# Kernel tuning notes

Measured on AMD Instinct MI355X. Metric: run time of the kernel, lower is better.

The kernel has to match this reference:

```python
import jax, jax.numpy as jnp
import numpy as np
from jax import lax

B, S, I, H = 16, 2048, 256, 512


def setup_inputs() -> dict:
    key = jax.random.key(0)
    k = jax.random.split(key, 5)
    s0 = 1.0 / np.sqrt(I + H)
    s1 = 1.0 / np.sqrt(H + H)
    return {
        "x": jax.random.normal(k[0], (B, S, I), dtype=jnp.float32),
        "W0": jax.random.uniform(k[1], (4 * H, I + H), minval=-s0, maxval=s0, dtype=jnp.float32),
        "b0": jax.random.uniform(k[2], (4 * H,), minval=-s0, maxval=s0, dtype=jnp.float32),
        "W1": jax.random.uniform(k[3], (4 * H, H + H), minval=-s1, maxval=s1, dtype=jnp.float32),
        "b1": jax.random.uniform(k[4], (4 * H,), minval=-s1, maxval=s1, dtype=jnp.float32),
    }


def _cell(xt, h, c, W, b):
    # gates: [B, 4H] = cat(xt, h) @ W^T + b
    g = jnp.concatenate([xt, h], axis=1) @ W.T + b
    i_t, f_t, c_tilde, o_t = jnp.split(g, 4, axis=1)
    c_new = jax.nn.sigmoid(f_t) * c + jax.nn.sigmoid(i_t) * jnp.tanh(c_tilde)
    h_new = jax.nn.sigmoid(o_t) * jnp.tanh(c_new)
    return h_new, c_new


def reference(x, W0, b0, W1, b1):
    b, s, _ = x.shape
    hdim = W0.shape[0] // 4
    z = jnp.zeros((b, hdim), dtype=x.dtype)
    init = (z, z, z, z)  # (h0, c0, h1, c1)

    def step(carry, xt):
        h0, c0, h1, c1 = carry
        h0, c0 = _cell(xt, h0, c0, W0, b0)
        h1, c1 = _cell(h0, h1, c1, W1, b1)
        return (h0, c0, h1, c1), h1

    (h0, c0, h1, c1), ys = lax.scan(step, init, jnp.swapaxes(x, 0, 1))
    outputs = jnp.swapaxes(ys, 0, 1)  # [B, S, H] (batch_first=True)
    h = jnp.stack([h0, h1], axis=0)  # [num_layers, B, H]
    c = jnp.stack([c0, c1], axis=0)
    return outputs, (h, c)
```

## Files before the change

### kernel.cpp

```cpp
#include <hip/hip_runtime.h>
#include <hip/hip_bf16.h>


#define BB 16
#define SS 2048
#define II 256
#define HH 512
#define NG0 32
#define NG1 32
#define BHH (BB * HH)
#define OUT_H_OFF (BB * SS * HH)
#define OUT_C_OFF (OUT_H_OFF + 2 * BB * HH)

typedef __bf16 bf16x8_t __attribute__((ext_vector_type(8)));
typedef float f32x4_t __attribute__((ext_vector_type(4)));

union b128u { uint64_t u[2]; bf16x8_t v; };

__device__ __forceinline__ float sigmoidf_(float x) { return 1.f / (1.f + __expf(-x)); }
__device__ __forceinline__ float tanhf_(float x) { return 1.f - 2.f / (__expf(2.f * x) + 1.f); }

__device__ __forceinline__ uint64_t cload64(const void* p) {
    return __hip_atomic_load((const uint64_t*)p, __ATOMIC_RELAXED, __HIP_MEMORY_SCOPE_AGENT);
}
__device__ __forceinline__ bf16x8_t cload_frag(const __bf16* p) {
    b128u r;
    r.u[0] = cload64(p);
    r.u[1] = cload64(p + 4);
    return r.v;
}
__device__ __forceinline__ void cstore_bf16(__bf16* p, float v) {
    __bf16 b = (__bf16)v;
    unsigned short u;
    __builtin_memcpy(&u, &b, 2);
    __hip_atomic_store((unsigned short*)p, u, __ATOMIC_RELAXED, __HIP_MEMORY_SCOPE_AGENT);
}

__device__ __forceinline__ void spin2(const int* f0, int T0, const int* f1, int T1) {
    const int lidx = threadIdx.x & 63;
    const int* p = (lidx < 32) ? (f0 + lidx) : (f1 + (lidx - 32));
    const int tgt = (lidx < 32) ? T0 : T1;
    while (true) {
        int v = __hip_atomic_load(p, __ATOMIC_RELAXED, __HIP_MEMORY_SCOPE_AGENT);
        if (__all(v >= tgt)) break;
    }
    __builtin_amdgcn_sched_barrier(0);
    asm volatile("" ::: "memory");
}

__device__ __forceinline__ bf16x8_t cvt8(const float* p) {
    f32x4_t a = *reinterpret_cast<const f32x4_t*>(p);
    f32x4_t b = *reinterpret_cast<const f32x4_t*>(p + 4);
    bf16x8_t r;
    r[0] = (__bf16)a[0]; r[1] = (__bf16)a[1];
    r[2] = (__bf16)a[2]; r[3] = (__bf16)a[3];
    r[4] = (__bf16)b[0]; r[5] = (__bf16)b[1];
    r[6] = (__bf16)b[2]; r[7] = (__bf16)b[3];
    return r;
}

#define MFMA(A, B, C) __builtin_amdgcn_mfma_f32_16x16x32_bf16((A), (B), (C), 0, 0, 0)

__global__ __launch_bounds__(256, 1) void lstm2_persistent(
    const float* __restrict__ x,
    const float* __restrict__ W0,
    const float* __restrict__ b0,
    const float* __restrict__ W1,
    const float* __restrict__ b1,
    float* __restrict__ out,
    int* flag0, int* flag1,
    __bf16* h0buf, __bf16* h1buf)
{
    const int tid = threadIdx.x;
    const int w   = tid >> 6;
    const int l   = tid & 63;
    const int cc  = l & 15;
    const int kg  = l >> 4;
    const int ew_b = tid >> 4;
    const int ew_u = tid & 15;

    __shared__ float gate_s[4][16][17];
    float cstate = 0.f;

    if (blockIdx.x < NG0) {
        const int blk   = blockIdx.x;
        const int ubase = blk * 16;
        const int gcol  = w * HH + ubase + cc;
        const float* wrow = W0 + (size_t)gcol * (II + HH);
        bf16x8_t wf[24];
#pragma unroll
        for (int kk = 0; kk < 24; ++kk)
            wf[kk] = cvt8(wrow + kk * 32 + kg * 8);
        const float bias  = b0[gcol];
        const float* xrow = x + (size_t)cc * SS * II;
        bf16x8_t xf[8];
#pragma unroll
        for (int kk = 0; kk < 8; ++kk)
            xf[kk] = cvt8(xrow + kk * 32 + kg * 8);
        __syncthreads();

        for (int t = 0; t < SS; ++t) {
            f32x4_t a0 = {0.f,0.f,0.f,0.f}, a1 = a0, a2 = a0, a3 = a0;
            a0 = MFMA(xf[0], wf[0], a0); a1 = MFMA(xf[1], wf[1], a1);
            a2 = MFMA(xf[2], wf[2], a2); a3 = MFMA(xf[3], wf[3], a3);
            a0 = MFMA(xf[4], wf[4], a0); a1 = MFMA(xf[5], wf[5], a1);
            a2 = MFMA(xf[6], wf[6], a2); a3 = MFMA(xf[7], wf[7], a3);

            spin2(flag0, t, flag1, t - 1);

            if (t > 0) {
                const __bf16* hp = h0buf + ((t - 1) & 1) * BHH + cc * HH + kg * 8;
#pragma unroll
                for (int kk = 0; kk < 16; kk += 4) {
                    a0 = MFMA(cload_frag(hp + (kk + 0) * 32), wf[8 + kk + 0], a0);
                    a1 = MFMA(cload_frag(hp + (kk + 1) * 32), wf[8 + kk + 1], a1);
                    a2 = MFMA(cload_frag(hp + (kk + 2) * 32), wf[8 + kk + 2], a2);
                    a3 = MFMA(cload_frag(hp + (kk + 3) * 32), wf[8 + kk + 3], a3);
                }
            }
            f32x4_t acc = (a0 + a1) + (a2 + a3);
#pragma unroll
            for (int r = 0; r < 4; ++r)
                gate_s[w][cc][kg * 4 + r] = acc[r] + bias;

            if (t + 1 < SS) {
                const float* xr = xrow + (size_t)(t + 1) * II;
#pragma unroll
                for (int kk = 0; kk < 8; ++kk)
                    xf[kk] = cvt8(xr + kk * 32 + kg * 8);
            }
            __syncthreads();
            {
                const float gi = gate_s[0][ew_u][ew_b];
                const float gf = gate_s[1][ew_u][ew_b];
                const float gg = gate_s[2][ew_u][ew_b];
                const float go = gate_s[3][ew_u][ew_b];
                const float cn = sigmoidf_(gf) * cstate + sigmoidf_(gi) * tanhf_(gg);
                const float hn = sigmoidf_(go) * tanhf_(cn);
                cstate = cn;
                cstore_bf16(h0buf + (t & 1) * BHH + ew_b * HH + ubase + ew_u, hn);
                if (t == SS - 1) {
                    out[OUT_H_OFF + ew_b * HH + ubase + ew_u] = hn;
                    out[OUT_C_OFF + ew_b * HH + ubase + ew_u] = cn;
                }
            }
            asm volatile("s_waitcnt vmcnt(0)" ::: "memory");
            __syncthreads();
            if (tid == 0)
                __hip_atomic_store(flag0 + blk, t + 1, __ATOMIC_RELAXED,
                                   __HIP_MEMORY_SCOPE_AGENT);
        }
    } else {
        const int blk   = blockIdx.x - NG0;
        const int ubase = blk * 16;
        const int gcol  = w * HH + ubase + cc;
        const float* wrow = W1 + (size_t)gcol * (2 * HH);
        bf16x8_t wf[32];
#pragma unroll
        for (int kk = 0; kk < 32; ++kk)
            wf[kk] = cvt8(wrow + kk * 32 + kg * 8);
        const float bias = b1[gcol];
        __syncthreads();

        for (int t = 0; t < SS; ++t) {
            f32x4_t a0 = {0.f,0.f,0.f,0.f}, a1 = a0, a2 = a0, a3 = a0;
            spin2(flag1, t, flag1, t);
            if (t > 0) {
                const __bf16* h1p = h1buf + ((t - 1) & 1) * BHH + cc * HH + kg * 8;
#pragma unroll
                for (int kk = 0; kk < 16; kk += 4) {
                    a0 = MFMA(cload_frag(h1p + (kk + 0) * 32), wf[16 + kk + 0], a0);
                    a1 = MFMA(cload_frag(h1p + (kk + 1) * 32), wf[16 + kk + 1], a1);
                    a2 = MFMA(cload_frag(h1p + (kk + 2) * 32), wf[16 + kk + 2], a2);
                    a3 = MFMA(cload_frag(h1p + (kk + 3) * 32), wf[16 + kk + 3], a3);
                }
            }
            spin2(flag0, t + 1, flag0, t + 1);
            {
                const __bf16* h0c = h0buf + (t & 1) * BHH + cc * HH + kg * 8;
#pragma unroll
                for (int kk = 0; kk < 16; kk += 4) {
                    a0 = MFMA(cload_frag(h0c + (kk + 0) * 32), wf[kk + 0], a0);
                    a1 = MFMA(cload_frag(h0c + (kk + 1) * 32), wf[kk + 1], a1);
                    a2 = MFMA(cload_frag(h0c + (kk + 2) * 32), wf[kk + 2], a2);
                    a3 = MFMA(cload_frag(h0c + (kk + 3) * 32), wf[kk + 3], a3);
                }
            }
            f32x4_t acc = (a0 + a1) + (a2 + a3);
#pragma unroll
            for (int r = 0; r < 4; ++r)
                gate_s[w][cc][kg * 4 + r] = acc[r] + bias;
            __syncthreads();
            {
                const float gi = gate_s[0][ew_u][ew_b];
                const float gf = gate_s[1][ew_u][ew_b];
                const float gg = gate_s[2][ew_u][ew_b];
                const float go = gate_s[3][ew_u][ew_b];
                const float cn = sigmoidf_(gf) * cstate + sigmoidf_(gi) * tanhf_(gg);
                const float hn = sigmoidf_(go) * tanhf_(cn);
                cstate = cn;
                cstore_bf16(h1buf + (t & 1) * BHH + ew_b * HH + ubase + ew_u, hn);
                out[((size_t)ew_b * SS + t) * HH + ubase + ew_u] = hn;
                if (t == SS - 1) {
                    out[OUT_H_OFF + (BB + ew_b) * HH + ubase + ew_u] = hn;
                    out[OUT_C_OFF + (BB + ew_b) * HH + ubase + ew_u] = cn;
                }
            }
            asm volatile("s_waitcnt vmcnt(0)" ::: "memory");
            __syncthreads();
            if (tid == 0)
                __hip_atomic_store(flag1 + blk, t + 1, __ATOMIC_RELAXED,
                                   __HIP_MEMORY_SCOPE_AGENT);
        }
    }
}

extern "C" void kernel_launch(void* const* d_in, const int* in_sizes, int n_in,
                              void* d_out, int out_size, void* d_ws, size_t ws_size,
                              hipStream_t stream) {
    const float* x  = (const float*)d_in[0];
    const float* W0 = (const float*)d_in[1];
    const float* b0 = (const float*)d_in[2];
    const float* W1 = (const float*)d_in[3];
    const float* b1 = (const float*)d_in[4];
    float* out = (float*)d_out;

    char* ws = (char*)d_ws;
    int* flag0 = (int*)ws;
    int* flag1 = (int*)(ws + 128);
    __bf16* h0buf = (__bf16*)(ws + 4096);
    __bf16* h1buf = (__bf16*)(ws + 4096 + 32768);

    hipMemsetAsync(ws, 0, 256, stream);

    hipLaunchKernelGGL(lstm2_persistent, dim3(NG0 + NG1), dim3(256), 0, stream,
                       x, W0, b0, W1, b1, out, flag0, flag1, h0buf, h1buf);
}
```

Measured before the change: 21.26 ms.

## Fuse both LSTM layers into one block per unit slice with skewed pipeline

Merges the layer-0 and layer-1 persistent blocks into 32 blocks of 512 threads. Waves 0-3 compute layer 0 at step t while waves 4-7 compute layer 1 at step t-1, so both layers share one grid-wide barrier per step instead of two dependent flag waits. Per-block flags are padded to separate cache lines and polled by one wave, and the next x load is issued before the spin and converted to bf16 afterwards to hide its latency. The price is a longer per-step critical path inside each block, since both layers' MFMA work and elementwise updates must finish before the block signals.

```diff
diff --git a/kernel.cpp b/kernel.cpp
--- a/kernel.cpp
+++ b/kernel.cpp
@@ -6,8 +6,7 @@
 #define SS 2048
 #define II 256
 #define HH 512
-#define NG0 32
-#define NG1 32
+#define NBLK 32
 #define BHH (BB * HH)
 #define OUT_H_OFF (BB * SS * HH)
 #define OUT_C_OFF (OUT_H_OFF + 2 * BB * HH)
@@ -36,21 +35,7 @@
     __hip_atomic_store((unsigned short*)p, u, __ATOMIC_RELAXED, __HIP_MEMORY_SCOPE_AGENT);
 }
 
-__device__ __forceinline__ void spin2(const int* f0, int T0, const int* f1, int T1) {
-    const int lidx = threadIdx.x & 63;
-    const int* p = (lidx < 32) ? (f0 + lidx) : (f1 + (lidx - 32));
-    const int tgt = (lidx < 32) ? T0 : T1;
-    while (true) {
-        int v = __hip_atomic_load(p, __ATOMIC_RELAXED, __HIP_MEMORY_SCOPE_AGENT);
-        if (__all(v >= tgt)) break;
-    }
-    __builtin_amdgcn_sched_barrier(0);
-    asm volatile("" ::: "memory");
-}
-
-__device__ __forceinline__ bf16x8_t cvt8(const float* p) {
-    f32x4_t a = *reinterpret_cast<const f32x4_t*>(p);
-    f32x4_t b = *reinterpret_cast<const f32x4_t*>(p + 4);
+__device__ __forceinline__ bf16x8_t pack8(f32x4_t a, f32x4_t b) {
     bf16x8_t r;
     r[0] = (__bf16)a[0]; r[1] = (__bf16)a[1];
     r[2] = (__bf16)a[2]; r[3] = (__bf16)a[3];
@@ -58,126 +43,129 @@
     r[6] = (__bf16)b[2]; r[7] = (__bf16)b[3];
     return r;
 }
+__device__ __forceinline__ bf16x8_t cvt8(const float* p) {
+    return pack8(*reinterpret_cast<const f32x4_t*>(p),
+                 *reinterpret_cast<const f32x4_t*>(p + 4));
+}
 
 #define MFMA(A, B, C) __builtin_amdgcn_mfma_f32_16x16x32_bf16((A), (B), (C), 0, 0, 0)
 
-__global__ __launch_bounds__(256, 1) void lstm2_persistent(
+__global__ __launch_bounds__(512, 1) void lstm2_fused(
     const float* __restrict__ x,
     const float* __restrict__ W0,
     const float* __restrict__ b0,
     const float* __restrict__ W1,
     const float* __restrict__ b1,
     float* __restrict__ out,
-    int* flag0, int* flag1,
+    int* flags,
     __bf16* h0buf, __bf16* h1buf)
 {
-    const int tid = threadIdx.x;
-    const int w   = tid >> 6;
-    const int l   = tid & 63;
-    const int cc  = l & 15;
-    const int kg  = l >> 4;
-    const int ew_b = tid >> 4;
-    const int ew_u = tid & 15;
-
-    __shared__ float gate_s[4][16][17];
-    float cstate = 0.f;
-
-    if (blockIdx.x < NG0) {
-        const int blk   = blockIdx.x;
-        const int ubase = blk * 16;
-        const int gcol  = w * HH + ubase + cc;
+    const int tid  = threadIdx.x;
+    const int w    = tid >> 6;
+    const int l    = tid & 63;
+    const int cc   = l & 15;
+    const int kg   = l >> 4;
+    const int gate = w & 3;
+    const bool isL0 = (w < 4);
+    const int blk   = blockIdx.x;
+    const int ubase = blk * 16;
+    const int gcol  = gate * HH + ubase + cc;
+
+    const int half = tid >> 8;
+    const int eb   = (tid >> 4) & 15;
+    const int eu   = tid & 15;
+
+    __shared__ float g0s[4][16][17];
+    __shared__ float g1s[4][16][17];
+
+    bf16x8_t wf[32];
+    float    bias;
+    bf16x8_t xf[8];
+    const float* xrow = x + (size_t)cc * SS * II;
+
+    if (isL0) {
         const float* wrow = W0 + (size_t)gcol * (II + HH);
-        bf16x8_t wf[24];
 #pragma unroll
         for (int kk = 0; kk < 24; ++kk)
             wf[kk] = cvt8(wrow + kk * 32 + kg * 8);
-        const float bias  = b0[gcol];
-        const float* xrow = x + (size_t)cc * SS * II;
-        bf16x8_t xf[8];
+        bias = b0[gcol];
 #pragma unroll
         for (int kk = 0; kk < 8; ++kk)
             xf[kk] = cvt8(xrow + kk * 32 + kg * 8);
-        __syncthreads();
-
-        for (int t = 0; t < SS; ++t) {
-            f32x4_t a0 = {0.f,0.f,0.f,0.f}, a1 = a0, a2 = a0, a3 = a0;
+    } else {
+        const float* wrow = W1 + (size_t)gcol * (2 * HH);
+#pragma unroll
+        for (int kk = 0; kk < 32; ++kk)
+            wf[kk] = cvt8(wrow + kk * 32 + kg * 8);
+        bias = b1[gcol];
+    }
+
+    float cstate = 0.f;
+    __syncthreads();
+
+    for (int t = 0; t <= SS; ++t) {
+        f32x4_t a0 = {0.f, 0.f, 0.f, 0.f}, a1 = a0, a2 = a0, a3 = a0;
+        f32x4_t xraw[16];
+
+        if (isL0 && t < SS) {
             a0 = MFMA(xf[0], wf[0], a0); a1 = MFMA(xf[1], wf[1], a1);
             a2 = MFMA(xf[2], wf[2], a2); a3 = MFMA(xf[3], wf[3], a3);
             a0 = MFMA(xf[4], wf[4], a0); a1 = MFMA(xf[5], wf[5], a1);
             a2 = MFMA(xf[6], wf[6], a2); a3 = MFMA(xf[7], wf[7], a3);
-
-            spin2(flag0, t, flag1, t - 1);
-
-            if (t > 0) {
-                const __bf16* hp = h0buf + ((t - 1) & 1) * BHH + cc * HH + kg * 8;
-#pragma unroll
-                for (int kk = 0; kk < 16; kk += 4) {
-                    a0 = MFMA(cload_frag(hp + (kk + 0) * 32), wf[8 + kk + 0], a0);
-                    a1 = MFMA(cload_frag(hp + (kk + 1) * 32), wf[8 + kk + 1], a1);
-                    a2 = MFMA(cload_frag(hp + (kk + 2) * 32), wf[8 + kk + 2], a2);
-                    a3 = MFMA(cload_frag(hp + (kk + 3) * 32), wf[8 + kk + 3], a3);
-                }
-            }
-            f32x4_t acc = (a0 + a1) + (a2 + a3);
-#pragma unroll
-            for (int r = 0; r < 4; ++r)
-                gate_s[w][cc][kg * 4 + r] = acc[r] + bias;
-
             if (t + 1 < SS) {
                 const float* xr = xrow + (size_t)(t + 1) * II;
 #pragma unroll
-                for (int kk = 0; kk < 8; ++kk)
-                    xf[kk] = cvt8(xr + kk * 32 + kg * 8);
-            }
-            __syncthreads();
-            {
-                const float gi = gate_s[0][ew_u][ew_b];
-                const float gf = gate_s[1][ew_u][ew_b];
-                const float gg = gate_s[2][ew_u][ew_b];
-                const float go = gate_s[3][ew_u][ew_b];
-                const float cn = sigmoidf_(gf) * cstate + sigmoidf_(gi) * tanhf_(gg);
-                const float hn = sigmoidf_(go) * tanhf_(cn);
-                cstate = cn;
-                cstore_bf16(h0buf + (t & 1) * BHH + ew_b * HH + ubase + ew_u, hn);
-                if (t == SS - 1) {
-                    out[OUT_H_OFF + ew_b * HH + ubase + ew_u] = hn;
-                    out[OUT_C_OFF + ew_b * HH + ubase + ew_u] = cn;
-                }
-            }
-            asm volatile("s_waitcnt vmcnt(0)" ::: "memory");
-            __syncthreads();
-            if (tid == 0)
-                __hip_atomic_store(flag0 + blk, t + 1, __ATOMIC_RELAXED,
-                                   __HIP_MEMORY_SCOPE_AGENT);
-        }
-    } else {
-        const int blk   = blockIdx.x - NG0;
-        const int ubase = blk * 16;
-        const int gcol  = w * HH + ubase + cc;
-        const float* wrow = W1 + (size_t)gcol * (2 * HH);
-        bf16x8_t wf[32];
-#pragma unroll
-        for (int kk = 0; kk < 32; ++kk)
-            wf[kk] = cvt8(wrow + kk * 32 + kg * 8);
-        const float bias = b1[gcol];
+                for (int kk = 0; kk < 8; ++kk) {
+                    xraw[2 * kk]     = *reinterpret_cast<const f32x4_t*>(xr + kk * 32 + kg * 8);
+                    xraw[2 * kk + 1] = *reinterpret_cast<const f32x4_t*>(xr + kk * 32 + kg * 8 + 4);
+                }
+            }
+        }
+
+        if (w == 0) {
+            const int* p = flags + (l & 31) * 32;
+            while (true) {
+                int v = __hip_atomic_load(p, __ATOMIC_RELAXED, __HIP_MEMORY_SCOPE_AGENT);
+                if (__all(v >= t)) break;
+            }
+        }
         __syncthreads();
 
-        for (int t = 0; t < SS; ++t) {
-            f32x4_t a0 = {0.f,0.f,0.f,0.f}, a1 = a0, a2 = a0, a3 = a0;
-            spin2(flag1, t, flag1, t);
-            if (t > 0) {
-                const __bf16* h1p = h1buf + ((t - 1) & 1) * BHH + cc * HH + kg * 8;
-#pragma unroll
-                for (int kk = 0; kk < 16; kk += 4) {
-                    a0 = MFMA(cload_frag(h1p + (kk + 0) * 32), wf[16 + kk + 0], a0);
-                    a1 = MFMA(cload_frag(h1p + (kk + 1) * 32), wf[16 + kk + 1], a1);
-                    a2 = MFMA(cload_frag(h1p + (kk + 2) * 32), wf[16 + kk + 2], a2);
-                    a3 = MFMA(cload_frag(h1p + (kk + 3) * 32), wf[16 + kk + 3], a3);
-                }
-            }
-            spin2(flag0, t + 1, flag0, t + 1);
-            {
-                const __bf16* h0c = h0buf + (t & 1) * BHH + cc * HH + kg * 8;
+        if (isL0) {
+            if (t < SS) {
+                if (t + 1 < SS) {
+#pragma unroll
+                    for (int kk = 0; kk < 8; ++kk)
+                        xf[kk] = pack8(xraw[2 * kk], xraw[2 * kk + 1]);
+                }
+                if (t > 0) {
+                    const __bf16* hp = h0buf + ((t - 1) & 1) * BHH + cc * HH + kg * 8;
+#pragma unroll
+                    for (int kk = 0; kk < 16; kk += 4) {
+                        a0 = MFMA(cload_frag(hp + (kk + 0) * 32), wf[8 + kk + 0], a0);
+                        a1 = MFMA(cload_frag(hp + (kk + 1) * 32), wf[8 + kk + 1], a1);
+                        a2 = MFMA(cload_frag(hp + (kk + 2) * 32), wf[8 + kk + 2], a2);
+                        a3 = MFMA(cload_frag(hp + (kk + 3) * 32), wf[8 + kk + 3], a3);
+                    }
+                }
+                f32x4_t acc = (a0 + a1) + (a2 + a3);
+#pragma unroll
+                for (int r = 0; r < 4; ++r)
+                    g0s[gate][cc][kg * 4 + r] = acc[r] + bias;
+            }
+        } else {
+            if (t >= 1) {
+                if (t >= 2) {
+                    const __bf16* h1p = h1buf + ((t - 2) & 1) * BHH + cc * HH + kg * 8;
+#pragma unroll
+                    for (int kk = 0; kk < 16; kk += 4) {
+                        a0 = MFMA(cload_frag(h1p + (kk + 0) * 32), wf[16 + kk + 0], a0);
+                        a1 = MFMA(cload_frag(h1p + (kk + 1) * 32), wf[16 + kk + 1], a1);
+                        a2 = MFMA(cload_frag(h1p + (kk + 2) * 32), wf[16 + kk + 2], a2);
+                        a3 = MFMA(cload_frag(h1p + (kk + 3) * 32), wf[16 + kk + 3], a3);
+                    }
+                }
+                const __bf16* h0c = h0buf + ((t - 1) & 1) * BHH + cc * HH + kg * 8;
 #pragma unroll
                 for (int kk = 0; kk < 16; kk += 4) {
                     a0 = MFMA(cload_frag(h0c + (kk + 0) * 32), wf[kk + 0], a0);
@@ -185,33 +173,52 @@
                     a2 = MFMA(cload_frag(h0c + (kk + 2) * 32), wf[kk + 2], a2);
                     a3 = MFMA(cload_frag(h0c + (kk + 3) * 32), wf[kk + 3], a3);
                 }
-            }
-            f32x4_t acc = (a0 + a1) + (a2 + a3);
-#pragma unroll
-            for (int r = 0; r < 4; ++r)
-                gate_s[w][cc][kg * 4 + r] = acc[r] + bias;
-            __syncthreads();
-            {
-                const float gi = gate_s[0][ew_u][ew_b];
-                const float gf = gate_s[1][ew_u][ew_b];
-                const float gg = gate_s[2][ew_u][ew_b];
-                const float go = gate_s[3][ew_u][ew_b];
+                f32x4_t acc = (a0 + a1) + (a2 + a3);
+#pragma unroll
+                for (int r = 0; r < 4; ++r)
+                    g1s[gate][cc][kg * 4 + r] = acc[r] + bias;
+            }
+        }
+        __syncthreads();
+
+        if (half == 0) {
+            if (t < SS) {
+                const float gi = g0s[0][eu][eb];
+                const float gf = g0s[1][eu][eb];
+                const float gg = g0s[2][eu][eb];
+                const float go = g0s[3][eu][eb];
                 const float cn = sigmoidf_(gf) * cstate + sigmoidf_(gi) * tanhf_(gg);
                 const float hn = sigmoidf_(go) * tanhf_(cn);
                 cstate = cn;
-                cstore_bf16(h1buf + (t & 1) * BHH + ew_b * HH + ubase + ew_u, hn);
-                out[((size_t)ew_b * SS + t) * HH + ubase + ew_u] = hn;
+                cstore_bf16(h0buf + (t & 1) * BHH + eb * HH + ubase + eu, hn);
                 if (t == SS - 1) {
-                    out[OUT_H_OFF + (BB + ew_b) * HH + ubase + ew_u] = hn;
-                    out[OUT_C_OFF + (BB + ew_b) * HH + ubase + ew_u] = cn;
-                }
-            }
-            asm volatile("s_waitcnt vmcnt(0)" ::: "memory");
-            __syncthreads();
-            if (tid == 0)
-                __hip_atomic_store(flag1 + blk, t + 1, __ATOMIC_RELAXED,
-                                   __HIP_MEMORY_SCOPE_AGENT);
-        }
+                    out[OUT_H_OFF + eb * HH + ubase + eu] = hn;
+                    out[OUT_C_OFF + eb * HH + ubase + eu] = cn;
+                }
+            }
+        } else {
+            if (t >= 1) {
+                const float gi = g1s[0][eu][eb];
+                const float gf = g1s[1][eu][eb];
+                const float gg = g1s[2][eu][eb];
+                const float go = g1s[3][eu][eb];
+                const float cn = sigmoidf_(gf) * cstate + sigmoidf_(gi) * tanhf_(gg);
+                const float hn = sigmoidf_(go) * tanhf_(cn);
+                cstate = cn;
+                cstore_bf16(h1buf + ((t - 1) & 1) * BHH + eb * HH + ubase + eu, hn);
+                out[((size_t)eb * SS + (t - 1)) * HH + ubase + eu] = hn;
+                if (t == SS) {
+                    out[OUT_H_OFF + (BB + eb) * HH + ubase + eu] = hn;
+                    out[OUT_C_OFF + (BB + eb) * HH + ubase + eu] = cn;
+                }
+            }
+        }
+
+        asm volatile("s_waitcnt vmcnt(0)" ::: "memory");
+        __syncthreads();
+        if (tid == 0)
+            __hip_atomic_store(flags + blk * 32, t + 1, __ATOMIC_RELAXED,
+                               __HIP_MEMORY_SCOPE_AGENT);
     }
 }
 
@@ -226,13 +233,12 @@
     float* out = (float*)d_out;
 
     char* ws = (char*)d_ws;
-    int* flag0 = (int*)ws;
-    int* flag1 = (int*)(ws + 128);
-    __bf16* h0buf = (__bf16*)(ws + 4096);
-    __bf16* h1buf = (__bf16*)(ws + 4096 + 32768);
-
-    hipMemsetAsync(ws, 0, 256, stream);
-
-    hipLaunchKernelGGL(lstm2_persistent, dim3(NG0 + NG1), dim3(256), 0, stream,
-                       x, W0, b0, W1, b1, out, flag0, flag1, h0buf, h1buf);
-}
+    int* flags = (int*)ws;
+    __bf16* h0buf = (__bf16*)(ws + 8192);
+    __bf16* h1buf = (__bf16*)(ws + 8192 + 32768);
+
+    hipMemsetAsync(ws, 0, 8192, stream);
+
+    hipLaunchKernelGGL(lstm2_fused, dim3(NBLK), dim3(512), 0, stream,
+                       x, W0, b0, W1, b1, out, flags, h0buf, h1buf);
+}
```

New measurement: 32.04 ms. +50.7%, slower.
